# Kernel optimization log

Hardware: AMD Instinct MI355X
Metric: run time of the kernel (lower is better)

Reference implementation:

```python
import jax, jax.numpy as jnp
import numpy as np
from jax import lax

B, T_ENCO, N_INP, N_HID, T_DECO = 1024, 128, 128, 256, 24


def _lin(x, W, b):
    return x @ W.T + b


def _lstm_cell(x, h, c, Wih, Whh, bih, bhh):
    # PyTorch LSTMCell gate order: input, forget, cell(g), output
    g = x @ Wih.T + bih + h @ Whh.T + bhh
    i, f, gg, o = jnp.split(g, 4, axis=-1)
    c2 = jax.nn.sigmoid(f) * c + jax.nn.sigmoid(i) * jnp.tanh(gg)
    return jax.nn.sigmoid(o) * jnp.tanh(c2), c2


def setup_inputs() -> dict:
    key = jax.random.key(0)
    ks = iter(jax.random.split(key, 48))
    def w(shape, s=0.05):
        return jax.random.normal(next(ks), shape, jnp.float32) * s
    m = N_HID
    return {
        "input_p_q": jax.random.normal(next(ks), (B, T_ENCO, N_INP), jnp.float32),
        "label_p": jax.random.normal(next(ks), (B, T_DECO), jnp.float32),
        "Ue_W": w((m, T_ENCO)), "Ue_b": w((m,)),
        "Ue2_W": w((m, N_INP)), "Ue2_b": w((m,)),
        "We_W": w((m, 2 * N_HID)), "We_b": w((m,)),
        "Ve_W": w((1, m)), "Ve_b": w((1,)),
        "Ud_W": w((N_HID, N_HID)), "Ud_b": w((N_HID,)),
        "Wd_W": w((N_HID, 2 * N_HID)), "Wd_b": w((N_HID,)),
        "Vd_W": w((1, N_HID)), "Vd_b": w((1,)),
        "enc_Wih": w((4 * N_HID, N_INP)), "enc_Whh": w((4 * N_HID, N_HID)),
        "enc_bih": w((4 * N_HID,)), "enc_bhh": w((4 * N_HID,)),
        "mid_Wih": w((4 * N_HID, N_HID)), "mid_Whh": w((4 * N_HID, N_HID)),
        "mid_bih": w((4 * N_HID,)), "mid_bhh": w((4 * N_HID,)),
        "dec_Wih": w((4 * N_HID, N_HID)), "dec_Whh": w((4 * N_HID, N_HID)),
        "dec_bih": w((4 * N_HID,)), "dec_bhh": w((4 * N_HID,)),
        "reg_W": w((1, N_HID)), "reg_b": w((1,)),
    }


def reference(input_p_q, label_p, Ue_W, Ue_b, Ue2_W, Ue2_b, We_W, We_b, Ve_W, Ve_b,
              Ud_W, Ud_b, Wd_W, Wd_b, Vd_W, Vd_b,
              enc_Wih, enc_Whh, enc_bih, enc_bhh,
              mid_Wih, mid_Whh, mid_bih, mid_bhh,
              dec_Wih, dec_Whh, dec_bih, dec_bhh,
              reg_W, reg_b):
    bsz = input_p_q.shape[0]
    inputs = input_p_q[:, :T_ENCO, :]                       # [B, T, n_inp]
    # Ue(inputs.transpose(1,2)) is loop-invariant: [B, n_inp, m]
    ue_x = _lin(jnp.swapaxes(inputs, 1, 2), Ue_W, Ue_b)
    z = jnp.zeros((bsz, N_HID), inputs.dtype)

    # --- spatial-attention encoder (LSTMCell over time) ---
    def enc_step(carry, x_i):                               # x_i: [B, n_inp]
        h, c = carry
        hc = _lin(jnp.concatenate([h, c], axis=1), We_W, We_b)[:, None, :]
        xi = _lin(x_i, Ue2_W, Ue2_b)[:, None, :]
        score = _lin(jnp.tanh(hc + ue_x + xi), Ve_W, Ve_b)[..., 0]  # [B, n_inp]
        a = jax.nn.softmax(score, axis=1)
        h2, c2 = _lstm_cell(x_i * a, h, c, enc_Wih, enc_Whh, enc_bih, enc_bhh)
        return (h2, c2), h2

    _, enc_hs = lax.scan(enc_step, (z, z), jnp.swapaxes(inputs, 0, 1))  # [T, B, H]

    # --- middle single-layer LSTM (zero init state) ---
    def mid_step(carry, x_t):
        h, c = carry
        h2, c2 = _lstm_cell(x_t, h, c, mid_Wih, mid_Whh, mid_bih, mid_bhh)
        return (h2, c2), h2

    _, mid = lax.scan(mid_step, (z, z), enc_hs)
    mid = jnp.swapaxes(mid, 0, 1)                            # [B, T, H]
    ud_mid = _lin(mid, Ud_W, Ud_b)                           # loop-invariant

    # --- temporal-attention decoder (note: raw (un-softmaxed) scores used in bmm,
    #     matching the original code) ---
    def dec_step(carry, _):
        hi, ci = carry
        wd = _lin(jnp.concatenate([hi, ci], axis=1), Wd_W, Wd_b)[:, None, :]
        t = _lin(jnp.tanh(wd + ud_mid), Vd_W, Vd_b)[..., 0]  # [B, T]
        dec_in = jnp.einsum('bt,bth->bh', t, mid)
        hi2, ci2 = _lstm_cell(dec_in, hi, ci, dec_Wih, dec_Whh, dec_bih, dec_bhh)
        return (hi2, ci2), hi2

    _, dec = lax.scan(dec_step, (z, z), None, length=T_DECO + 6)
    dec = jnp.swapaxes(dec, 0, 1)                            # [B, T_deco+6, H]
    out = _lin(dec, reg_W, reg_b)[..., 0]                    # [B, T_deco+6]
    return out[:, -T_DECO:]
```

## Files before the change

### kernel.cpp

```cpp
#include <hip/hip_runtime.h>


#define B_   1024
#define T_   128
#define NI_  128
#define H_   256
#define H4_  1024
#define TD_  24
#define DS_  30
#define BB   4
#define TB   1024

typedef _Float16 hf_t;
typedef _Float16 half8  __attribute__((ext_vector_type(8)));
typedef _Float16 half2v __attribute__((ext_vector_type(2)));

__device__ __forceinline__ float sigm(float x) {
    return __builtin_amdgcn_rcpf(1.0f + __expf(-x));
}
__device__ __forceinline__ float tanh_f(float x) {
    float e = __expf(2.0f * x);
    return 1.0f - 2.0f * __builtin_amdgcn_rcpf(e + 1.0f);
}
__device__ __forceinline__ float fdot2f(half2v a, half2v b, float c) {
#if __has_builtin(__builtin_amdgcn_fdot2)
    return __builtin_amdgcn_fdot2(a, b, c, false);
#else
    return fmaf((float)a.x, (float)b.x, fmaf((float)a.y, (float)b.y, c));
#endif
}
__device__ __forceinline__ float dot8h(half8 w, half8 x, float acc) {
    acc = fdot2f(__builtin_shufflevector(w, w, 0, 1), __builtin_shufflevector(x, x, 0, 1), acc);
    acc = fdot2f(__builtin_shufflevector(w, w, 2, 3), __builtin_shufflevector(x, x, 2, 3), acc);
    acc = fdot2f(__builtin_shufflevector(w, w, 4, 5), __builtin_shufflevector(x, x, 4, 5), acc);
    acc = fdot2f(__builtin_shufflevector(w, w, 6, 7), __builtin_shufflevector(x, x, 6, 7), acc);
    return acc;
}
__device__ __forceinline__ hf_t nt_load_h(const hf_t* p) {
#if __has_builtin(__builtin_nontemporal_load)
    return __builtin_nontemporal_load(p);
#else
    return *p;
#endif
}
__device__ __forceinline__ void nt_store_h(hf_t v, hf_t* p) {
#if __has_builtin(__builtin_nontemporal_store)
    __builtin_nontemporal_store(v, p);
#else
    *p = v;
#endif
}

#define W_WE    0u
#define W_UE2   131072u
#define W_EWIH  163840u
#define W_EWHH  294912u
#define W_MWIH  557056u
#define W_MWHH  819200u
#define W_DWIH  1081344u
#define W_DWHH  1343488u
#define W_WD    1605632u
#define W_UD    1736704u
#define SCR_A   2097152u
#define SCR_B   35651584u

__global__ void convw_kernel(const float* __restrict__ sWE, const float* __restrict__ sUE2,
                             const float* __restrict__ sEI, const float* __restrict__ sEH,
                             const float* __restrict__ sMI, const float* __restrict__ sMH,
                             const float* __restrict__ sDI, const float* __restrict__ sDH,
                             const float* __restrict__ sWD, const float* __restrict__ sUD,
                             hf_t* __restrict__ dst) {
    const int gtid = blockIdx.x * blockDim.x + threadIdx.x;
    const int gs   = gridDim.x * blockDim.x;
    for (int n = gtid; n < 131072; n += gs) {
        int e = n & 7, q = n >> 3, k = q & 255, c = q >> 8, kq = c >> 4, i = c & 15;
        dst[W_WE + n] = (hf_t)sWE[k * 512 + kq * 128 + i * 8 + e];
    }
    for (int n = gtid; n < 32768; n += gs) {
        int e = n & 7, q = n >> 3, k = q & 255, c = q >> 8, kq = c >> 2, i = c & 3;
        dst[W_UE2 + n] = (hf_t)sUE2[k * 128 + kq * 32 + i * 8 + e];
    }
    for (int n = gtid; n < 131072; n += gs) {
        int e = n & 7, q = n >> 3, o = q & 1023, i = q >> 10;
        dst[W_EWIH + n] = (hf_t)sEI[o * 128 + i * 8 + e];
    }
    for (int n = gtid; n < 262144; n += gs) {
        int e = n & 7, q = n >> 3, o = q & 1023, i = q >> 10;
        int s = o * 256 + i * 8 + e;
        dst[W_EWHH + n] = (hf_t)sEH[s];
        dst[W_MWIH + n] = (hf_t)sMI[s];
        dst[W_MWHH + n] = (hf_t)sMH[s];
        dst[W_DWIH + n] = (hf_t)sDI[s];
        dst[W_DWHH + n] = (hf_t)sDH[s];
    }
    for (int n = gtid; n < 131072; n += gs) {
        int e = n & 7, q = n >> 3, k = q & 255, c = q >> 8, kq = c >> 4, i = c & 15;
        dst[W_WD + n] = (hf_t)sWD[k * 512 + kq * 128 + i * 8 + e];
    }
    for (int n = gtid; n < 65536; n += gs)
        dst[W_UD + n] = (hf_t)sUD[n];
}

#define O_HC    0
#define O_CF    1024
#define O_HM    2048
#define O_CMF   2560
#define O_XRAW  3584
#define O_XH    4096
#define O_XG    4352
#define O_HCXI  4608
#define O_SPART 5632
#define O_SBUF  6656
#define O_GBUF  7168
#define O_DINH  11264
#define O_HF    11776
#define O_VES   12800
#define O_VDS   13056

__global__ __launch_bounds__(TB, 4) void dsrnn_kernel(
    const float* __restrict__ inp,
    const float* __restrict__ UeW,  const float* __restrict__ Ueb,
    const float* __restrict__ Ue2b,
    const float* __restrict__ Web,
    const float* __restrict__ VeW,  const float* __restrict__ Veb,
    const float* __restrict__ Udb,
    const float* __restrict__ Wdb,
    const float* __restrict__ VdW,  const float* __restrict__ Vdb,
    const float* __restrict__ ebih, const float* __restrict__ ebhh,
    const float* __restrict__ mbih, const float* __restrict__ mbhh,
    const float* __restrict__ dbih, const float* __restrict__ dbhh,
    const float* __restrict__ rW,   const float* __restrict__ rb,
    const hf_t* __restrict__ wb,
    hf_t* __restrict__ scrA,
    hf_t* __restrict__ scrB,
    float* __restrict__ out)
{
    __shared__ float sm[16384];
    const int tid = threadIdx.x;
    const int b0  = blockIdx.x * BB;

    hf_t*  hc   = (hf_t*)(sm + O_HC);
    float* cf   = sm + O_CF;
    hf_t*  hm   = (hf_t*)(sm + O_HM);
    float* cmf  = sm + O_CMF;
    float* xraw = sm + O_XRAW;
    hf_t*  xh   = (hf_t*)(sm + O_XH);
    hf_t*  xg   = (hf_t*)(sm + O_XG);
    float* hcxi = sm + O_HCXI;
    float* spart= sm + O_SPART;
    float* sbuf = sm + O_SBUF;
    float* gbuf = sm + O_GBUF;
    hf_t*  dinh = (hf_t*)(sm + O_DINH);
    float* hful = sm + O_HF;
    float* ves  = sm + O_VES;
    float* vds  = sm + O_VDS;

    {
        const int j = tid & 127, kq8 = tid >> 7;
        for (int b = 0; b < BB; ++b) {
            __syncthreads();
            const float* Xg = inp + (size_t)(b0 + b) * T_ * NI_;
            for (int i = tid; i < T_ * NI_; i += TB) sm[i] = Xg[i];
            __syncthreads();
            hf_t* ub = scrA + (size_t)(b0 + b) * H_ * NI_;
            for (int k = kq8 * 32; k < kq8 * 32 + 32; ++k) {
                const float* wrow = UeW + (size_t)k * T_;
                float acc = Ueb[k];
#pragma unroll 4
                for (int t = 0; t < T_; ++t) acc = fmaf(wrow[t], sm[t * NI_ + j], acc);
                nt_store_h((hf_t)acc, ub + (size_t)k * NI_ + j);
            }
        }
    }
    __syncthreads();
    for (int i = tid; i < 3584; i += TB) sm[i] = 0.0f;
    if (tid < 256) { ves[tid] = VeW[tid]; vds[tid] = VdW[tid]; }
    __syncthreads();

    for (int t = 0; t < T_; ++t) {
        if (tid < 512) {
            const int b = tid >> 7, j = tid & 127;
            float v = inp[((size_t)(b0 + b) * T_ + t) * NI_ + j];
            xraw[b * NI_ + j] = v;
            xh[b * NI_ + j]   = (hf_t)v;
        }
        __syncthreads();

        {
            const int k = tid & 255, kq = tid >> 8;
            const half8* wWE = (const half8*)(wb + W_WE)  + (size_t)(kq * 16) * 256 + k;
            const half8* wU2 = (const half8*)(wb + W_UE2) + (size_t)(kq * 4)  * 256 + k;
            float a0 = 0.f, a1 = 0.f, a2 = 0.f, a3 = 0.f;
#pragma unroll 8
            for (int i = 0; i < 16; ++i) {
                half8 w = wWE[(size_t)i * 256];
                a0 = dot8h(w, *(const half8*)&hc[0 * 512 + kq * 128 + i * 8], a0);
                a1 = dot8h(w, *(const half8*)&hc[1 * 512 + kq * 128 + i * 8], a1);
                a2 = dot8h(w, *(const half8*)&hc[2 * 512 + kq * 128 + i * 8], a2);
                a3 = dot8h(w, *(const half8*)&hc[3 * 512 + kq * 128 + i * 8], a3);
            }
#pragma unroll
            for (int i = 0; i < 4; ++i) {
                half8 w = wU2[(size_t)i * 256];
                a0 = dot8h(w, *(const half8*)&xh[0 * 128 + kq * 32 + i * 8], a0);
                a1 = dot8h(w, *(const half8*)&xh[1 * 128 + kq * 32 + i * 8], a1);
                a2 = dot8h(w, *(const half8*)&xh[2 * 128 + kq * 32 + i * 8], a2);
                a3 = dot8h(w, *(const half8*)&xh[3 * 128 + kq * 32 + i * 8], a3);
            }
            gbuf[kq * 1024 + 0 * 256 + k] = a0;
            gbuf[kq * 1024 + 1 * 256 + k] = a1;
            gbuf[kq * 1024 + 2 * 256 + k] = a2;
            gbuf[kq * 1024 + 3 * 256 + k] = a3;
        }
        __syncthreads();
        {
            const int b = tid >> 8, k = tid & 255;
            hcxi[b * 256 + k] = gbuf[b * 256 + k] + gbuf[1024 + b * 256 + k]
                              + gbuf[2048 + b * 256 + k] + gbuf[3072 + b * 256 + k]
                              + Web[k] + Ue2b[k];
        }
        __syncthreads();

        {
            const int b = tid >> 8, r = tid & 255, kh = r >> 7, j = r & 127;
            const hf_t* up = scrA + ((size_t)(b0 + b) * 256 + kh * 128) * 128 + j;
            const float* hx = hcxi + b * 256 + kh * 128;
            const float* vw = ves + kh * 128;
            float acc = kh ? 0.f : Veb[0];
#pragma unroll 8
            for (int k2 = 0; k2 < 128; ++k2) {
                float u = (float)nt_load_h(up + (size_t)k2 * 128);
                acc = fmaf(vw[k2], tanh_f(hx[k2] + u), acc);
            }
            spart[tid] = acc;
        }
        __syncthreads();

        if (tid < 256) {
            const int b = tid >> 6, lane = tid & 63;
            const int base = b << 8;
            float sA = spart[base + lane]      + spart[base + 128 + lane];
            float sB = spart[base + 64 + lane] + spart[base + 192 + lane];
            float m = fmaxf(sA, sB);
            for (int d = 1; d < 64; d <<= 1) m = fmaxf(m, __shfl_xor(m, d));
            float eA = __expf(sA - m), eB = __expf(sB - m);
            float ssum = eA + eB;
            for (int d = 1; d < 64; d <<= 1) ssum += __shfl_xor(ssum, d);
            float inv = 1.0f / ssum;
            xg[b * NI_ + lane]      = (hf_t)(xraw[b * NI_ + lane] * eA * inv);
            xg[b * NI_ + lane + 64] = (hf_t)(xraw[b * NI_ + lane + 64] * eB * inv);
        }
        __syncthreads();

        {
            const int o = tid;
            const half8* wih = (const half8*)(wb + W_EWIH) + o;
            const half8* whh = (const half8*)(wb + W_EWHH) + o;
            float bias = ebih[o] + ebhh[o];
            float a0 = bias, a1 = bias, a2 = bias, a3 = bias;
#pragma unroll 8
            for (int i = 0; i < 16; ++i) {
                half8 w = wih[(size_t)i * 1024];
                a0 = dot8h(w, *(const half8*)&xg[0 * 128 + i * 8], a0);
                a1 = dot8h(w, *(const half8*)&xg[1 * 128 + i * 8], a1);
                a2 = dot8h(w, *(const half8*)&xg[2 * 128 + i * 8], a2);
                a3 = dot8h(w, *(const half8*)&xg[3 * 128 + i * 8], a3);
            }
#pragma unroll 8
            for (int i = 0; i < 32; ++i) {
                half8 w = whh[(size_t)i * 1024];
                a0 = dot8h(w, *(const half8*)&hc[0 * 512 + i * 8], a0);
                a1 = dot8h(w, *(const half8*)&hc[1 * 512 + i * 8], a1);
                a2 = dot8h(w, *(const half8*)&hc[2 * 512 + i * 8], a2);
                a3 = dot8h(w, *(const half8*)&hc[3 * 512 + i * 8], a3);
            }
            gbuf[0 * 1024 + o] = a0; gbuf[1 * 1024 + o] = a1;
            gbuf[2 * 1024 + o] = a2; gbuf[3 * 1024 + o] = a3;
        }
        __syncthreads();

        {
            const int b = tid >> 8, k = tid & 255;
            float gi = gbuf[b * H4_ + k];
            float gf = gbuf[b * H4_ + H_ + k];
            float gg = gbuf[b * H4_ + 2 * H_ + k];
            float go = gbuf[b * H4_ + 3 * H_ + k];
            float c2 = sigm(gf) * cf[b * H_ + k] + sigm(gi) * tanh_f(gg);
            float h2 = sigm(go) * tanh_f(c2);
            cf[b * H_ + k] = c2;
            hc[b * 512 + k]       = (hf_t)h2;
            hc[b * 512 + 256 + k] = (hf_t)c2;
        }
        __syncthreads();

        {
            const int o = tid;
            const half8* wih = (const half8*)(wb + W_MWIH) + o;
            const half8* whh = (const half8*)(wb + W_MWHH) + o;
            float bias = mbih[o] + mbhh[o];
            float a0 = bias, a1 = bias, a2 = bias, a3 = bias;
#pragma unroll 8
            for (int i = 0; i < 32; ++i) {
                half8 w = wih[(size_t)i * 1024];
                a0 = dot8h(w, *(const half8*)&hc[0 * 512 + i * 8], a0);
                a1 = dot8h(w, *(const half8*)&hc[1 * 512 + i * 8], a1);
                a2 = dot8h(w, *(const half8*)&hc[2 * 512 + i * 8], a2);
                a3 = dot8h(w, *(const half8*)&hc[3 * 512 + i * 8], a3);
            }
#pragma unroll 8
            for (int i = 0; i < 32; ++i) {
                half8 w = whh[(size_t)i * 1024];
                a0 = dot8h(w, *(const half8*)&hm[0 * 256 + i * 8], a0);
                a1 = dot8h(w, *(const half8*)&hm[1 * 256 + i * 8], a1);
                a2 = dot8h(w, *(const half8*)&hm[2 * 256 + i * 8], a2);
                a3 = dot8h(w, *(const half8*)&hm[3 * 256 + i * 8], a3);
            }
            gbuf[0 * 1024 + o] = a0; gbuf[1 * 1024 + o] = a1;
            gbuf[2 * 1024 + o] = a2; gbuf[3 * 1024 + o] = a3;
        }
        __syncthreads();

        {
            const int b = tid >> 8, k = tid & 255;
            float gi = gbuf[b * H4_ + k];
            float gf = gbuf[b * H4_ + H_ + k];
            float gg = gbuf[b * H4_ + 2 * H_ + k];
            float go = gbuf[b * H4_ + 3 * H_ + k];
            float c2 = sigm(gf) * cmf[b * H_ + k] + sigm(gi) * tanh_f(gg);
            float h2 = sigm(go) * tanh_f(c2);
            cmf[b * H_ + k] = c2;
            hm[b * 256 + k] = (hf_t)h2;
            scrB[((size_t)(b0 + b) * T_ + t) * H_ + k] = (hf_t)h2;
        }
        __syncthreads();
    }

    {
        const int b = tid >> 8, r = tid & 255, oh = r >> 7, tt = r & 127;
        const half8* mrow = (const half8*)(scrB + ((size_t)(b0 + b) * T_ + tt) * H_);
        half8 m[32];
#pragma unroll
        for (int i = 0; i < 32; ++i) m[i] = mrow[i];
        const half8* udw = (const half8*)(wb + W_UD);
        for (int o2 = 0; o2 < 128; ++o2) {
            const int o = oh * 128 + o2;
            const half8* ur = udw + (size_t)o * 32;
            float acc = Udb[o];
#pragma unroll 8
            for (int i = 0; i < 32; ++i) acc = dot8h(ur[i], m[i], acc);
            nt_store_h((hf_t)acc, scrA + ((size_t)(b0 + b) * 256 + o) * 128 + tt);
        }
    }
    __syncthreads();
    for (int i = tid; i < 2048; i += TB) sm[i] = 0.0f;
    __syncthreads();

    for (int s = 0; s < DS_; ++s) {
        {
            const int k = tid & 255, kq = tid >> 8;
            const half8* wWD = (const half8*)(wb + W_WD) + (size_t)(kq * 16) * 256 + k;
            float a0 = 0.f, a1 = 0.f, a2 = 0.f, a3 = 0.f;
#pragma unroll 8
            for (int i = 0; i < 16; ++i) {
                half8 w = wWD[(size_t)i * 256];
                a0 = dot8h(w, *(const half8*)&hc[0 * 512 + kq * 128 + i * 8], a0);
                a1 = dot8h(w, *(const half8*)&hc[1 * 512 + kq * 128 + i * 8], a1);
                a2 = dot8h(w, *(const half8*)&hc[2 * 512 + kq * 128 + i * 8], a2);
                a3 = dot8h(w, *(const half8*)&hc[3 * 512 + kq * 128 + i * 8], a3);
            }
            gbuf[kq * 1024 + 0 * 256 + k] = a0;
            gbuf[kq * 1024 + 1 * 256 + k] = a1;
            gbuf[kq * 1024 + 2 * 256 + k] = a2;
            gbuf[kq * 1024 + 3 * 256 + k] = a3;
        }
        __syncthreads();
        {
            const int b = tid >> 8, k = tid & 255;
            hcxi[b * 256 + k] = gbuf[b * 256 + k] + gbuf[1024 + b * 256 + k]
                              + gbuf[2048 + b * 256 + k] + gbuf[3072 + b * 256 + k]
                              + Wdb[k];
        }
        __syncthreads();

        {
            const int b = tid >> 8, r = tid & 255, kh = r >> 7, j = r & 127;
            const hf_t* up = scrA + ((size_t)(b0 + b) * 256 + kh * 128) * 128 + j;
            const float* hx = hcxi + b * 256 + kh * 128;
            const float* vw = vds + kh * 128;
            float acc = kh ? 0.f : Vdb[0];
#pragma unroll 8
            for (int k2 = 0; k2 < 128; ++k2) {
                float u = (float)nt_load_h(up + (size_t)k2 * 128);
                acc = fmaf(vw[k2], tanh_f(hx[k2] + u), acc);
            }
            spart[tid] = acc;
        }
        __syncthreads();
        if (tid < 512) {
            const int b = tid >> 7, j = tid & 127;
            sbuf[b * T_ + j] = spart[(b << 8) + j] + spart[(b << 8) + 128 + j];
        }
        __syncthreads();

        {
            const int b = tid >> 8, h = tid & 255;
            const hf_t* mp = scrB + (size_t)(b0 + b) * T_ * H_ + h;
            float acc = 0.0f;
            for (int j = 0; j < T_; ++j)
                acc = fmaf(sbuf[b * T_ + j], (float)mp[(size_t)j * H_], acc);
            dinh[b * 256 + h] = (hf_t)acc;
        }
        __syncthreads();

        {
            const int o = tid;
            const half8* wih = (const half8*)(wb + W_DWIH) + o;
            const half8* whh = (const half8*)(wb + W_DWHH) + o;
            float bias = dbih[o] + dbhh[o];
            float a0 = bias, a1 = bias, a2 = bias, a3 = bias;
#pragma unroll 8
            for (int i = 0; i < 32; ++i) {
                half8 w = wih[(size_t)i * 1024];
                a0 = dot8h(w, *(const half8*)&dinh[0 * 256 + i * 8], a0);
                a1 = dot8h(w, *(const half8*)&dinh[1 * 256 + i * 8], a1);
                a2 = dot8h(w, *(const half8*)&dinh[2 * 256 + i * 8], a2);
                a3 = dot8h(w, *(const half8*)&dinh[3 * 256 + i * 8], a3);
            }
#pragma unroll 8
            for (int i = 0; i < 32; ++i) {
                half8 w = whh[(size_t)i * 1024];
                a0 = dot8h(w, *(const half8*)&hc[0 * 512 + i * 8], a0);
                a1 = dot8h(w, *(const half8*)&hc[1 * 512 + i * 8], a1);
                a2 = dot8h(w, *(const half8*)&hc[2 * 512 + i * 8], a2);
                a3 = dot8h(w, *(const half8*)&hc[3 * 512 + i * 8], a3);
            }
            gbuf[0 * 1024 + o] = a0; gbuf[1 * 1024 + o] = a1;
            gbuf[2 * 1024 + o] = a2; gbuf[3 * 1024 + o] = a3;
        }
        __syncthreads();

        {
            const int b = tid >> 8, k = tid & 255;
            float gi = gbuf[b * H4_ + k];
            float gf = gbuf[b * H4_ + H_ + k];
            float gg = gbuf[b * H4_ + 2 * H_ + k];
            float go = gbuf[b * H4_ + 3 * H_ + k];
            float c2 = sigm(gf) * cf[b * H_ + k] + sigm(gi) * tanh_f(gg);
            float h2 = sigm(go) * tanh_f(c2);
            cf[b * H_ + k] = c2;
            hc[b * 512 + k]       = (hf_t)h2;
            hc[b * 512 + 256 + k] = (hf_t)c2;
            hful[b * H_ + k] = h2;
        }
        __syncthreads();

        if (s >= 6 && tid < 256) {
            const int b = tid >> 6, lane = tid & 63;
            float p = rW[lane]       * hful[b * H_ + lane]
                    + rW[lane + 64]  * hful[b * H_ + lane + 64]
                    + rW[lane + 128] * hful[b * H_ + lane + 128]
                    + rW[lane + 192] * hful[b * H_ + lane + 192];
            for (int d = 1; d < 64; d <<= 1) p += __shfl_xor(p, d);
            if (lane == 0) out[(size_t)(b0 + b) * TD_ + (s - 6)] = p + rb[0];
        }
        __syncthreads();
    }
}

extern "C" void kernel_launch(void* const* d_in, const int* in_sizes, int n_in,
                              void* d_out, int out_size, void* d_ws, size_t ws_size,
                              hipStream_t stream) {
    const float* inp  = (const float*)d_in[0];
    const float* UeW  = (const float*)d_in[2];
    const float* Ueb  = (const float*)d_in[3];
    const float* Ue2W = (const float*)d_in[4];
    const float* Ue2b = (const float*)d_in[5];
    const float* WeW  = (const float*)d_in[6];
    const float* Web  = (const float*)d_in[7];
    const float* VeW  = (const float*)d_in[8];
    const float* Veb  = (const float*)d_in[9];
    const float* UdW  = (const float*)d_in[10];
    const float* Udb  = (const float*)d_in[11];
    const float* WdW  = (const float*)d_in[12];
    const float* Wdb  = (const float*)d_in[13];
    const float* VdW  = (const float*)d_in[14];
    const float* Vdb  = (const float*)d_in[15];
    const float* eWih = (const float*)d_in[16];
    const float* eWhh = (const float*)d_in[17];
    const float* ebih = (const float*)d_in[18];
    const float* ebhh = (const float*)d_in[19];
    const float* mWih = (const float*)d_in[20];
    const float* mWhh = (const float*)d_in[21];
    const float* mbih = (const float*)d_in[22];
    const float* mbhh = (const float*)d_in[23];
    const float* dWih = (const float*)d_in[24];
    const float* dWhh = (const float*)d_in[25];
    const float* dbih = (const float*)d_in[26];
    const float* dbhh = (const float*)d_in[27];
    const float* rW   = (const float*)d_in[28];
    const float* rb   = (const float*)d_in[29];

    hf_t* wsb  = (hf_t*)d_ws;
    hf_t* scrA = wsb + SCR_A;
    hf_t* scrB = wsb + SCR_B;

    convw_kernel<<<512, 256, 0, stream>>>(WeW, Ue2W, eWih, eWhh, mWih, mWhh,
                                          dWih, dWhh, WdW, UdW, wsb);

    dsrnn_kernel<<<B_ / BB, TB, 0, stream>>>(
        inp, UeW, Ueb, Ue2b, Web, VeW, Veb, Udb, Wdb, VdW, Vdb,
        ebih, ebhh, mbih, mbhh, dbih, dbhh, rW, rb,
        wsb, scrA, scrB, (float*)d_out);
}
```

Measured before the change: 10.75 ms.

## Halve per-block batch to two rows and repartition thread work

Cuts the batch rows per block from four to two, which doubles the grid to 512 blocks and halves shared memory. The launch-bounds hint rises so more blocks can be resident per CU. Attention-score, context and Ud loops are split across more threads with extra partial-sum reductions, so all 1024 threads stay busy on half the data. The cost is that each weight load from global/L2 is now reused by only two batch rows instead of four, roughly doubling total weight traffic.

```diff
diff --git a/kernel.cpp b/kernel.cpp
--- a/kernel.cpp
+++ b/kernel.cpp
@@ -8,7 +8,7 @@
 #define H4_  1024
 #define TD_  24
 #define DS_  30
-#define BB   4
+#define BB   2
 #define TB   1024
 
 typedef _Float16 hf_t;
@@ -102,22 +102,22 @@
 }
 
 #define O_HC    0
-#define O_CF    1024
-#define O_HM    2048
-#define O_CMF   2560
-#define O_XRAW  3584
-#define O_XH    4096
-#define O_XG    4352
-#define O_HCXI  4608
-#define O_SPART 5632
-#define O_SBUF  6656
-#define O_GBUF  7168
-#define O_DINH  11264
-#define O_HF    11776
-#define O_VES   12800
-#define O_VDS   13056
-
-__global__ __launch_bounds__(TB, 4) void dsrnn_kernel(
+#define O_CF    512
+#define O_HM    1024
+#define O_CMF   1280
+#define O_XRAW  1792
+#define O_XH    2048
+#define O_XG    2176
+#define O_HCXI  2304
+#define O_SPART 2816
+#define O_SBUF  3840
+#define O_GBUF  4096
+#define O_DINH  6144
+#define O_HF    6400
+#define O_VES   6912
+#define O_VDS   7168
+
+__global__ __launch_bounds__(TB, 8) void dsrnn_kernel(
     const float* __restrict__ inp,
     const float* __restrict__ UeW,  const float* __restrict__ Ueb,
     const float* __restrict__ Ue2b,
@@ -135,7 +135,7 @@
     hf_t* __restrict__ scrB,
     float* __restrict__ out)
 {
-    __shared__ float sm[16384];
+    __shared__ float sm[8192];
     const int tid = threadIdx.x;
     const int b0  = blockIdx.x * BB;
 
@@ -156,29 +156,36 @@
     float* vds  = sm + O_VDS;
 
     {
-        const int j = tid & 127, kq8 = tid >> 7;
+        const int jj = tid & 63;
+        const int kg = tid >> 6;
         for (int b = 0; b < BB; ++b) {
-            __syncthreads();
             const float* Xg = inp + (size_t)(b0 + b) * T_ * NI_;
-            for (int i = tid; i < T_ * NI_; i += TB) sm[i] = Xg[i];
-            __syncthreads();
             hf_t* ub = scrA + (size_t)(b0 + b) * H_ * NI_;
-            for (int k = kq8 * 32; k < kq8 * 32 + 32; ++k) {
-                const float* wrow = UeW + (size_t)k * T_;
-                float acc = Ueb[k];
+            for (int jh = 0; jh < 2; ++jh) {
+                __syncthreads();
+                for (int i = tid; i < 128 * 64; i += TB) {
+                    int t = i >> 6, j2 = i & 63;
+                    sm[i] = Xg[t * NI_ + jh * 64 + j2];
+                }
+                __syncthreads();
+                const int j = jh * 64 + jj;
+                for (int k = kg * 16; k < kg * 16 + 16; ++k) {
+                    const float* wrow = UeW + (size_t)k * T_;
+                    float acc = Ueb[k];
 #pragma unroll 4
-                for (int t = 0; t < T_; ++t) acc = fmaf(wrow[t], sm[t * NI_ + j], acc);
-                nt_store_h((hf_t)acc, ub + (size_t)k * NI_ + j);
+                    for (int t = 0; t < T_; ++t) acc = fmaf(wrow[t], sm[t * 64 + jj], acc);
+                    nt_store_h((hf_t)acc, ub + (size_t)k * NI_ + j);
+                }
             }
         }
     }
     __syncthreads();
-    for (int i = tid; i < 3584; i += TB) sm[i] = 0.0f;
+    for (int i = tid; i < 2048; i += TB) sm[i] = 0.0f;
     if (tid < 256) { ves[tid] = VeW[tid]; vds[tid] = VdW[tid]; }
     __syncthreads();
 
     for (int t = 0; t < T_; ++t) {
-        if (tid < 512) {
+        if (tid < 256) {
             const int b = tid >> 7, j = tid & 127;
             float v = inp[((size_t)(b0 + b) * T_ + t) * NI_ + j];
             xraw[b * NI_ + j] = v;
@@ -190,45 +197,39 @@
             const int k = tid & 255, kq = tid >> 8;
             const half8* wWE = (const half8*)(wb + W_WE)  + (size_t)(kq * 16) * 256 + k;
             const half8* wU2 = (const half8*)(wb + W_UE2) + (size_t)(kq * 4)  * 256 + k;
-            float a0 = 0.f, a1 = 0.f, a2 = 0.f, a3 = 0.f;
+            float a0 = 0.f, a1 = 0.f;
 #pragma unroll 8
             for (int i = 0; i < 16; ++i) {
                 half8 w = wWE[(size_t)i * 256];
                 a0 = dot8h(w, *(const half8*)&hc[0 * 512 + kq * 128 + i * 8], a0);
                 a1 = dot8h(w, *(const half8*)&hc[1 * 512 + kq * 128 + i * 8], a1);
-                a2 = dot8h(w, *(const half8*)&hc[2 * 512 + kq * 128 + i * 8], a2);
-                a3 = dot8h(w, *(const half8*)&hc[3 * 512 + kq * 128 + i * 8], a3);
             }
 #pragma unroll
             for (int i = 0; i < 4; ++i) {
                 half8 w = wU2[(size_t)i * 256];
                 a0 = dot8h(w, *(const half8*)&xh[0 * 128 + kq * 32 + i * 8], a0);
                 a1 = dot8h(w, *(const half8*)&xh[1 * 128 + kq * 32 + i * 8], a1);
-                a2 = dot8h(w, *(const half8*)&xh[2 * 128 + kq * 32 + i * 8], a2);
-                a3 = dot8h(w, *(const half8*)&xh[3 * 128 + kq * 32 + i * 8], a3);
-            }
-            gbuf[kq * 1024 + 0 * 256 + k] = a0;
-            gbuf[kq * 1024 + 1 * 256 + k] = a1;
-            gbuf[kq * 1024 + 2 * 256 + k] = a2;
-            gbuf[kq * 1024 + 3 * 256 + k] = a3;
-        }
-        __syncthreads();
-        {
+            }
+            gbuf[kq * 512 + 0 * 256 + k] = a0;
+            gbuf[kq * 512 + 1 * 256 + k] = a1;
+        }
+        __syncthreads();
+        if (tid < 512) {
             const int b = tid >> 8, k = tid & 255;
-            hcxi[b * 256 + k] = gbuf[b * 256 + k] + gbuf[1024 + b * 256 + k]
-                              + gbuf[2048 + b * 256 + k] + gbuf[3072 + b * 256 + k]
+            hcxi[b * 256 + k] = gbuf[b * 256 + k] + gbuf[512 + b * 256 + k]
+                              + gbuf[1024 + b * 256 + k] + gbuf[1536 + b * 256 + k]
                               + Web[k] + Ue2b[k];
         }
         __syncthreads();
 
         {
-            const int b = tid >> 8, r = tid & 255, kh = r >> 7, j = r & 127;
-            const hf_t* up = scrA + ((size_t)(b0 + b) * 256 + kh * 128) * 128 + j;
-            const float* hx = hcxi + b * 256 + kh * 128;
-            const float* vw = ves + kh * 128;
-            float acc = kh ? 0.f : Veb[0];
-#pragma unroll 8
-            for (int k2 = 0; k2 < 128; ++k2) {
+            const int b = tid >> 9, kq = (tid >> 7) & 3, j = tid & 127;
+            const hf_t* up = scrA + ((size_t)(b0 + b) * 256 + kq * 64) * 128 + j;
+            const float* hx = hcxi + b * 256 + kq * 64;
+            const float* vw = ves + kq * 64;
+            float acc = (kq == 0) ? Veb[0] : 0.f;
+#pragma unroll 8
+            for (int k2 = 0; k2 < 64; ++k2) {
                 float u = (float)nt_load_h(up + (size_t)k2 * 128);
                 acc = fmaf(vw[k2], tanh_f(hx[k2] + u), acc);
             }
@@ -236,11 +237,13 @@
         }
         __syncthreads();
 
-        if (tid < 256) {
+        if (tid < 128) {
             const int b = tid >> 6, lane = tid & 63;
-            const int base = b << 8;
-            float sA = spart[base + lane]      + spart[base + 128 + lane];
-            float sB = spart[base + 64 + lane] + spart[base + 192 + lane];
+            const int base = b << 9;
+            float sA = spart[base + lane]       + spart[base + 128 + lane]
+                     + spart[base + 256 + lane] + spart[base + 384 + lane];
+            float sB = spart[base + 64 + lane]  + spart[base + 192 + lane]
+                     + spart[base + 320 + lane] + spart[base + 448 + lane];
             float m = fmaxf(sA, sB);
             for (int d = 1; d < 64; d <<= 1) m = fmaxf(m, __shfl_xor(m, d));
             float eA = __expf(sA - m), eB = __expf(sB - m);
@@ -257,29 +260,24 @@
             const half8* wih = (const half8*)(wb + W_EWIH) + o;
             const half8* whh = (const half8*)(wb + W_EWHH) + o;
             float bias = ebih[o] + ebhh[o];
-            float a0 = bias, a1 = bias, a2 = bias, a3 = bias;
+            float a0 = bias, a1 = bias;
 #pragma unroll 8
             for (int i = 0; i < 16; ++i) {
                 half8 w = wih[(size_t)i * 1024];
                 a0 = dot8h(w, *(const half8*)&xg[0 * 128 + i * 8], a0);
                 a1 = dot8h(w, *(const half8*)&xg[1 * 128 + i * 8], a1);
-                a2 = dot8h(w, *(const half8*)&xg[2 * 128 + i * 8], a2);
-                a3 = dot8h(w, *(const half8*)&xg[3 * 128 + i * 8], a3);
             }
 #pragma unroll 8
             for (int i = 0; i < 32; ++i) {
                 half8 w = whh[(size_t)i * 1024];
                 a0 = dot8h(w, *(const half8*)&hc[0 * 512 + i * 8], a0);
                 a1 = dot8h(w, *(const half8*)&hc[1 * 512 + i * 8], a1);
-                a2 = dot8h(w, *(const half8*)&hc[2 * 512 + i * 8], a2);
-                a3 = dot8h(w, *(const half8*)&hc[3 * 512 + i * 8], a3);
             }
             gbuf[0 * 1024 + o] = a0; gbuf[1 * 1024 + o] = a1;
-            gbuf[2 * 1024 + o] = a2; gbuf[3 * 1024 + o] = a3;
-        }
-        __syncthreads();
-
-        {
+        }
+        __syncthreads();
+
+        if (tid < 512) {
             const int b = tid >> 8, k = tid & 255;
             float gi = gbuf[b * H4_ + k];
             float gf = gbuf[b * H4_ + H_ + k];
@@ -298,29 +296,24 @@
             const half8* wih = (const half8*)(wb + W_MWIH) + o;
             const half8* whh = (const half8*)(wb + W_MWHH) + o;
             float bias = mbih[o] + mbhh[o];
-            float a0 = bias, a1 = bias, a2 = bias, a3 = bias;
+            float a0 = bias, a1 = bias;
 #pragma unroll 8
             for (int i = 0; i < 32; ++i) {
                 half8 w = wih[(size_t)i * 1024];
                 a0 = dot8h(w, *(const half8*)&hc[0 * 512 + i * 8], a0);
                 a1 = dot8h(w, *(const half8*)&hc[1 * 512 + i * 8], a1);
-                a2 = dot8h(w, *(const half8*)&hc[2 * 512 + i * 8], a2);
-                a3 = dot8h(w, *(const half8*)&hc[3 * 512 + i * 8], a3);
             }
 #pragma unroll 8
             for (int i = 0; i < 32; ++i) {
                 half8 w = whh[(size_t)i * 1024];
                 a0 = dot8h(w, *(const half8*)&hm[0 * 256 + i * 8], a0);
                 a1 = dot8h(w, *(const half8*)&hm[1 * 256 + i * 8], a1);
-                a2 = dot8h(w, *(const half8*)&hm[2 * 256 + i * 8], a2);
-                a3 = dot8h(w, *(const half8*)&hm[3 * 256 + i * 8], a3);
             }
             gbuf[0 * 1024 + o] = a0; gbuf[1 * 1024 + o] = a1;
-            gbuf[2 * 1024 + o] = a2; gbuf[3 * 1024 + o] = a3;
-        }
-        __syncthreads();
-
-        {
+        }
+        __syncthreads();
+
+        if (tid < 512) {
             const int b = tid >> 8, k = tid & 255;
             float gi = gbuf[b * H4_ + k];
             float gf = gbuf[b * H4_ + H_ + k];
@@ -336,14 +329,14 @@
     }
 
     {
-        const int b = tid >> 8, r = tid & 255, oh = r >> 7, tt = r & 127;
+        const int b = tid >> 9, r = tid & 511, oq = r >> 7, tt = r & 127;
         const half8* mrow = (const half8*)(scrB + ((size_t)(b0 + b) * T_ + tt) * H_);
         half8 m[32];
 #pragma unroll
         for (int i = 0; i < 32; ++i) m[i] = mrow[i];
         const half8* udw = (const half8*)(wb + W_UD);
-        for (int o2 = 0; o2 < 128; ++o2) {
-            const int o = oh * 128 + o2;
+        for (int o2 = 0; o2 < 64; ++o2) {
+            const int o = oq * 64 + o2;
             const half8* ur = udw + (size_t)o * 32;
             float acc = Udb[o];
 #pragma unroll 8
@@ -352,63 +345,67 @@
         }
     }
     __syncthreads();
-    for (int i = tid; i < 2048; i += TB) sm[i] = 0.0f;
+    for (int i = tid; i < 1024; i += TB) sm[i] = 0.0f;
     __syncthreads();
 
     for (int s = 0; s < DS_; ++s) {
         {
             const int k = tid & 255, kq = tid >> 8;
             const half8* wWD = (const half8*)(wb + W_WD) + (size_t)(kq * 16) * 256 + k;
-            float a0 = 0.f, a1 = 0.f, a2 = 0.f, a3 = 0.f;
+            float a0 = 0.f, a1 = 0.f;
 #pragma unroll 8
             for (int i = 0; i < 16; ++i) {
                 half8 w = wWD[(size_t)i * 256];
                 a0 = dot8h(w, *(const half8*)&hc[0 * 512 + kq * 128 + i * 8], a0);
                 a1 = dot8h(w, *(const half8*)&hc[1 * 512 + kq * 128 + i * 8], a1);
-                a2 = dot8h(w, *(const half8*)&hc[2 * 512 + kq * 128 + i * 8], a2);
-                a3 = dot8h(w, *(const half8*)&hc[3 * 512 + kq * 128 + i * 8], a3);
-            }
-            gbuf[kq * 1024 + 0 * 256 + k] = a0;
-            gbuf[kq * 1024 + 1 * 256 + k] = a1;
-            gbuf[kq * 1024 + 2 * 256 + k] = a2;
-            gbuf[kq * 1024 + 3 * 256 + k] = a3;
-        }
-        __syncthreads();
-        {
+            }
+            gbuf[kq * 512 + 0 * 256 + k] = a0;
+            gbuf[kq * 512 + 1 * 256 + k] = a1;
+        }
+        __syncthreads();
+        if (tid < 512) {
             const int b = tid >> 8, k = tid & 255;
-            hcxi[b * 256 + k] = gbuf[b * 256 + k] + gbuf[1024 + b * 256 + k]
-                              + gbuf[2048 + b * 256 + k] + gbuf[3072 + b * 256 + k]
+            hcxi[b * 256 + k] = gbuf[b * 256 + k] + gbuf[512 + b * 256 + k]
+                              + gbuf[1024 + b * 256 + k] + gbuf[1536 + b * 256 + k]
                               + Wdb[k];
         }
         __syncthreads();
 
         {
-            const int b = tid >> 8, r = tid & 255, kh = r >> 7, j = r & 127;
-            const hf_t* up = scrA + ((size_t)(b0 + b) * 256 + kh * 128) * 128 + j;
-            const float* hx = hcxi + b * 256 + kh * 128;
-            const float* vw = vds + kh * 128;
-            float acc = kh ? 0.f : Vdb[0];
-#pragma unroll 8
-            for (int k2 = 0; k2 < 128; ++k2) {
+            const int b = tid >> 9, kq = (tid >> 7) & 3, j = tid & 127;
+            const hf_t* up = scrA + ((size_t)(b0 + b) * 256 + kq * 64) * 128 + j;
+            const float* hx = hcxi + b * 256 + kq * 64;
+            const float* vw = vds + kq * 64;
+            float acc = (kq == 0) ? Vdb[0] : 0.f;
+#pragma unroll 8
+            for (int k2 = 0; k2 < 64; ++k2) {
                 float u = (float)nt_load_h(up + (size_t)k2 * 128);
                 acc = fmaf(vw[k2], tanh_f(hx[k2] + u), acc);
             }
             spart[tid] = acc;
         }
         __syncthreads();
-        if (tid < 512) {
+        if (tid < 256) {
             const int b = tid >> 7, j = tid & 127;
-            sbuf[b * T_ + j] = spart[(b << 8) + j] + spart[(b << 8) + 128 + j];
-        }
-        __syncthreads();
-
-        {
-            const int b = tid >> 8, h = tid & 255;
+            const int base = b << 9;
+            sbuf[b * T_ + j] = spart[base + j] + spart[base + 128 + j]
+                             + spart[base + 256 + j] + spart[base + 384 + j];
+        }
+        __syncthreads();
+
+        {
+            const int b = tid >> 9, jh = (tid >> 8) & 1, h = tid & 255;
             const hf_t* mp = scrB + (size_t)(b0 + b) * T_ * H_ + h;
             float acc = 0.0f;
-            for (int j = 0; j < T_; ++j)
-                acc = fmaf(sbuf[b * T_ + j], (float)mp[(size_t)j * H_], acc);
-            dinh[b * 256 + h] = (hf_t)acc;
+            const int jbase = jh * 64;
+            for (int j = 0; j < 64; ++j)
+                acc = fmaf(sbuf[b * T_ + jbase + j], (float)mp[(size_t)(jbase + j) * H_], acc);
+            gbuf[(b * 2 + jh) * 256 + h] = acc;
+        }
+        __syncthreads();
+        if (tid < 512) {
+            const int b = tid >> 8, h = tid & 255;
+            dinh[b * 256 + h] = (hf_t)(gbuf[b * 512 + h] + gbuf[b * 512 + 256 + h]);
         }
         __syncthreads();
 
@@ -417,29 +414,24 @@
             const half8* wih = (const half8*)(wb + W_DWIH) + o;
             const half8* whh = (const half8*)(wb + W_DWHH) + o;
             float bias = dbih[o] + dbhh[o];
-            float a0 = bias, a1 = bias, a2 = bias, a3 = bias;
+            float a0 = bias, a1 = bias;
 #pragma unroll 8
             for (int i = 0; i < 32; ++i) {
                 half8 w = wih[(size_t)i * 1024];
                 a0 = dot8h(w, *(const half8*)&dinh[0 * 256 + i * 8], a0);
                 a1 = dot8h(w, *(const half8*)&dinh[1 * 256 + i * 8], a1);
-                a2 = dot8h(w, *(const half8*)&dinh[2 * 256 + i * 8], a2);
-                a3 = dot8h(w, *(const half8*)&dinh[3 * 256 + i * 8], a3);
             }
 #pragma unroll 8
             for (int i = 0; i < 32; ++i) {
                 half8 w = whh[(size_t)i * 1024];
                 a0 = dot8h(w, *(const half8*)&hc[0 * 512 + i * 8], a0);
                 a1 = dot8h(w, *(const half8*)&hc[1 * 512 + i * 8], a1);
-                a2 = dot8h(w, *(const half8*)&hc[2 * 512 + i * 8], a2);
-                a3 = dot8h(w, *(const half8*)&hc[3 * 512 + i * 8], a3);
             }
             gbuf[0 * 1024 + o] = a0; gbuf[1 * 1024 + o] = a1;
-            gbuf[2 * 1024 + o] = a2; gbuf[3 * 1024 + o] = a3;
-        }
-        __syncthreads();
-
-        {
+        }
+        __syncthreads();
+
+        if (tid < 512) {
             const int b = tid >> 8, k = tid & 255;
             float gi = gbuf[b * H4_ + k];
             float gf = gbuf[b * H4_ + H_ + k];
@@ -454,7 +446,7 @@
         }
         __syncthreads();
 
-        if (s >= 6 && tid < 256) {
+        if (s >= 6 && tid < 128) {
             const int b = tid >> 6, lane = tid & 63;
             float p = rW[lane]       * hful[b * H_ + lane]
                     + rW[lane + 64]  * hful[b * H_ + lane + 64]
```

New measurement: 16.71 ms. 55.4% more time.

## Vectorize attention score and context loads with half8 and split-K partial sums

Applied to the files above, without the earlier changes.

The encoder spatial-attention and decoder temporal-attention score loops are rewritten so each thread loads eight fp16 values at once along j and covers a 16-wide slice of k, instead of scalar strided loads across all 128 k. Partial sums go to a new shared buffer and a second pass reduces them. The decoder context bmm over mid gets the same half8-vector, split-over-time treatment with an extra reduction pass. The aim is fewer, wider global memory transactions and more independent tanh/FMA chains per thread, at the cost of more shared memory, an extra barrier and a different reduction order.

```diff
diff --git a/kernel.cpp b/kernel.cpp
--- a/kernel.cpp
+++ b/kernel.cpp
@@ -37,6 +37,13 @@
     return acc;
 }
 __device__ __forceinline__ hf_t nt_load_h(const hf_t* p) {
+#if __has_builtin(__builtin_nontemporal_load)
+    return __builtin_nontemporal_load(p);
+#else
+    return *p;
+#endif
+}
+__device__ __forceinline__ half8 nt_load_h8(const half8* p) {
 #if __has_builtin(__builtin_nontemporal_load)
     return __builtin_nontemporal_load(p);
 #else
@@ -109,13 +116,13 @@
 #define O_XH    4096
 #define O_XG    4352
 #define O_HCXI  4608
-#define O_SPART 5632
 #define O_SBUF  6656
 #define O_GBUF  7168
-#define O_DINH  11264
+#define O_SP2   7168
 #define O_HF    11776
-#define O_VES   12800
-#define O_VDS   13056
+#define O_VES   15360
+#define O_VDS   15616
+#define O_DINH  15872
 
 __global__ __launch_bounds__(TB, 4) void dsrnn_kernel(
     const float* __restrict__ inp,
@@ -147,9 +154,9 @@
     hf_t*  xh   = (hf_t*)(sm + O_XH);
     hf_t*  xg   = (hf_t*)(sm + O_XG);
     float* hcxi = sm + O_HCXI;
-    float* spart= sm + O_SPART;
     float* sbuf = sm + O_SBUF;
     float* gbuf = sm + O_GBUF;
+    float* sp2  = sm + O_SP2;
     hf_t*  dinh = (hf_t*)(sm + O_DINH);
     float* hful = sm + O_HF;
     float* ves  = sm + O_VES;
@@ -222,25 +229,39 @@
         __syncthreads();
 
         {
-            const int b = tid >> 8, r = tid & 255, kh = r >> 7, j = r & 127;
-            const hf_t* up = scrA + ((size_t)(b0 + b) * 256 + kh * 128) * 128 + j;
-            const float* hx = hcxi + b * 256 + kh * 128;
-            const float* vw = ves + kh * 128;
-            float acc = kh ? 0.f : Veb[0];
-#pragma unroll 8
-            for (int k2 = 0; k2 < 128; ++k2) {
-                float u = (float)nt_load_h(up + (size_t)k2 * 128);
-                acc = fmaf(vw[k2], tanh_f(hx[k2] + u), acc);
-            }
-            spart[tid] = acc;
+            const int jv = tid & 15, kg = (tid >> 4) & 15, b = tid >> 8;
+            const hf_t* up = scrA + ((size_t)(b0 + b) * 256 + kg * 16) * 128 + jv * 8;
+            const float* hx = hcxi + b * 256 + kg * 16;
+            const float* vw = ves + kg * 16;
+            float ac0 = 0.f, ac1 = 0.f, ac2 = 0.f, ac3 = 0.f;
+            float ac4 = 0.f, ac5 = 0.f, ac6 = 0.f, ac7 = 0.f;
+#pragma unroll 4
+            for (int kk = 0; kk < 16; ++kk) {
+                half8 u = nt_load_h8((const half8*)(up + (size_t)kk * 128));
+                float hv = hx[kk], vv = vw[kk];
+                ac0 = fmaf(vv, tanh_f(hv + (float)u[0]), ac0);
+                ac1 = fmaf(vv, tanh_f(hv + (float)u[1]), ac1);
+                ac2 = fmaf(vv, tanh_f(hv + (float)u[2]), ac2);
+                ac3 = fmaf(vv, tanh_f(hv + (float)u[3]), ac3);
+                ac4 = fmaf(vv, tanh_f(hv + (float)u[4]), ac4);
+                ac5 = fmaf(vv, tanh_f(hv + (float)u[5]), ac5);
+                ac6 = fmaf(vv, tanh_f(hv + (float)u[6]), ac6);
+                ac7 = fmaf(vv, tanh_f(hv + (float)u[7]), ac7);
+            }
+            float* dst = sp2 + (b * 16 + kg) * 128 + jv * 8;
+            dst[0] = ac0; dst[1] = ac1; dst[2] = ac2; dst[3] = ac3;
+            dst[4] = ac4; dst[5] = ac5; dst[6] = ac6; dst[7] = ac7;
         }
         __syncthreads();
 
         if (tid < 256) {
             const int b = tid >> 6, lane = tid & 63;
-            const int base = b << 8;
-            float sA = spart[base + lane]      + spart[base + 128 + lane];
-            float sB = spart[base + 64 + lane] + spart[base + 192 + lane];
+            float sA = 0.f, sB = 0.f;
+#pragma unroll
+            for (int kg = 0; kg < 16; ++kg) {
+                sA += sp2[(b * 16 + kg) * 128 + lane];
+                sB += sp2[(b * 16 + kg) * 128 + lane + 64];
+            }
             float m = fmaxf(sA, sB);
             for (int d = 1; d < 64; d <<= 1) m = fmaxf(m, __shfl_xor(m, d));
             float eA = __expf(sA - m), eB = __expf(sB - m);
@@ -383,32 +404,69 @@
         __syncthreads();
 
         {
-            const int b = tid >> 8, r = tid & 255, kh = r >> 7, j = r & 127;
-            const hf_t* up = scrA + ((size_t)(b0 + b) * 256 + kh * 128) * 128 + j;
-            const float* hx = hcxi + b * 256 + kh * 128;
-            const float* vw = vds + kh * 128;
-            float acc = kh ? 0.f : Vdb[0];
-#pragma unroll 8
-            for (int k2 = 0; k2 < 128; ++k2) {
-                float u = (float)nt_load_h(up + (size_t)k2 * 128);
-                acc = fmaf(vw[k2], tanh_f(hx[k2] + u), acc);
-            }
-            spart[tid] = acc;
+            const int jv = tid & 15, kg = (tid >> 4) & 15, b = tid >> 8;
+            const hf_t* up = scrA + ((size_t)(b0 + b) * 256 + kg * 16) * 128 + jv * 8;
+            const float* hx = hcxi + b * 256 + kg * 16;
+            const float* vw = vds + kg * 16;
+            float ac0 = 0.f, ac1 = 0.f, ac2 = 0.f, ac3 = 0.f;
+            float ac4 = 0.f, ac5 = 0.f, ac6 = 0.f, ac7 = 0.f;
+#pragma unroll 4
+            for (int kk = 0; kk < 16; ++kk) {
+                half8 u = nt_load_h8((const half8*)(up + (size_t)kk * 128));
+                float hv = hx[kk], vv = vw[kk];
+                ac0 = fmaf(vv, tanh_f(hv + (float)u[0]), ac0);
+                ac1 = fmaf(vv, tanh_f(hv + (float)u[1]), ac1);
+                ac2 = fmaf(vv, tanh_f(hv + (float)u[2]), ac2);
+                ac3 = fmaf(vv, tanh_f(hv + (float)u[3]), ac3);
+                ac4 = fmaf(vv, tanh_f(hv + (float)u[4]), ac4);
+                ac5 = fmaf(vv, tanh_f(hv + (float)u[5]), ac5);
+                ac6 = fmaf(vv, tanh_f(hv + (float)u[6]), ac6);
+                ac7 = fmaf(vv, tanh_f(hv + (float)u[7]), ac7);
+            }
+            float* dst = sp2 + (b * 16 + kg) * 128 + jv * 8;
+            dst[0] = ac0; dst[1] = ac1; dst[2] = ac2; dst[3] = ac3;
+            dst[4] = ac4; dst[5] = ac5; dst[6] = ac6; dst[7] = ac7;
         }
         __syncthreads();
         if (tid < 512) {
             const int b = tid >> 7, j = tid & 127;
-            sbuf[b * T_ + j] = spart[(b << 8) + j] + spart[(b << 8) + 128 + j];
-        }
-        __syncthreads();
-
+            float sacc = Vdb[0];
+#pragma unroll
+            for (int kg = 0; kg < 16; ++kg) sacc += sp2[(b * 16 + kg) * 128 + j];
+            sbuf[b * T_ + j] = sacc;
+        }
+        __syncthreads();
+
+        {
+            const int hv = tid & 31, jg = (tid >> 5) & 7, b = tid >> 8;
+            const hf_t* mp = scrB + ((size_t)(b0 + b) * T_ + jg * 16) * H_ + hv * 8;
+            const float* sb = sbuf + b * T_ + jg * 16;
+            float ac0 = 0.f, ac1 = 0.f, ac2 = 0.f, ac3 = 0.f;
+            float ac4 = 0.f, ac5 = 0.f, ac6 = 0.f, ac7 = 0.f;
+#pragma unroll 4
+            for (int jj = 0; jj < 16; ++jj) {
+                half8 m = *(const half8*)(mp + (size_t)jj * H_);
+                float sv = sb[jj];
+                ac0 = fmaf(sv, (float)m[0], ac0);
+                ac1 = fmaf(sv, (float)m[1], ac1);
+                ac2 = fmaf(sv, (float)m[2], ac2);
+                ac3 = fmaf(sv, (float)m[3], ac3);
+                ac4 = fmaf(sv, (float)m[4], ac4);
+                ac5 = fmaf(sv, (float)m[5], ac5);
+                ac6 = fmaf(sv, (float)m[6], ac6);
+                ac7 = fmaf(sv, (float)m[7], ac7);
+            }
+            float* dst = sp2 + (b * 8 + jg) * 256 + hv * 8;
+            dst[0] = ac0; dst[1] = ac1; dst[2] = ac2; dst[3] = ac3;
+            dst[4] = ac4; dst[5] = ac5; dst[6] = ac6; dst[7] = ac7;
+        }
+        __syncthreads();
         {
             const int b = tid >> 8, h = tid & 255;
-            const hf_t* mp = scrB + (size_t)(b0 + b) * T_ * H_ + h;
-            float acc = 0.0f;
-            for (int j = 0; j < T_; ++j)
-                acc = fmaf(sbuf[b * T_ + j], (float)mp[(size_t)j * H_], acc);
-            dinh[b * 256 + h] = (hf_t)acc;
+            float sacc = 0.f;
+#pragma unroll
+            for (int jg = 0; jg < 8; ++jg) sacc += sp2[(b * 8 + jg) * 256 + h];
+            dinh[b * 256 + h] = (hf_t)sacc;
         }
         __syncthreads();
 
```

Result: no change. 10.69 ms (-0.6%).
